# Optimization experiments

Hardware: AMD Instinct MI355X
Metric: run time of the kernel (lower is better)

## Reference

```python
import jax, jax.numpy as jnp
import numpy as np

B, V_IN, V_OUT, F_IN, F_OUT, N_CP = 100000, 128, 128, 512, 512, 16
DIM_H = max(V_IN, V_OUT)  # hidden_vectors=None -> max(dim_vectors_in, dim_vectors_out)
EPS = 1e-8


def setup_inputs() -> dict:
    key = jax.random.key(0)
    ks = jax.random.split(key, 9)
    u = lambda k, shape, scale: jax.random.uniform(k, shape, jnp.float32, -scale, scale)
    wh_k = 1.0 / np.sqrt(V_IN).astype(np.float32)
    wu_k = 1.0 / np.sqrt(DIM_H + N_CP).astype(np.float32)
    f_in = DIM_H + N_CP + F_IN  # 656
    kf = 1.0 / np.sqrt(f_in).astype(np.float32)
    kg = 1.0 / np.sqrt(F_OUT).astype(np.float32)
    return {
        "feats": jax.random.normal(ks[0], (B, F_IN), jnp.float32),
        "vectors": jax.random.normal(ks[1], (B, V_IN, 3), jnp.float32),
        "Wh": u(ks[2], (V_IN, DIM_H), wh_k),
        "Wcp": u(ks[3], (V_IN, 2 * N_CP), wh_k),
        "Wu": u(ks[4], (DIM_H + N_CP, V_OUT), wu_k),
        "Wf": u(ks[5], (f_in, F_OUT), kf),      # torch Linear weight, stored (in,out)
        "bf": u(ks[6], (F_OUT,), kf),
        "Wg": u(ks[7], (F_OUT, V_OUT), kg),
        "bg": u(ks[8], (V_OUT,), kg),
    }


def reference(feats, vectors, Wh, Wcp, Wu, Wf, bf, Wg, bg):
    # vectors: [b, v_in, 3]; mix vector channels (matmul acts per xyz component c)
    Vh = jnp.einsum('bvc,vh->bhc', vectors, Wh)            # [b, dim_h, 3]
    # cross-product features
    Vcp = jnp.einsum('bvc,vp->bpc', vectors, Wcp)          # [b, 2*n_cp, 3]
    cp = jnp.cross(Vcp[:, :N_CP], Vcp[:, N_CP:])           # [b, n_cp, 3]
    Vh = jnp.concatenate([Vh, cp], axis=1)                 # [b, dim_h+n_cp, 3]
    Vu = jnp.einsum('bkc,ko->boc', Vh, Wu)                 # [b, v_out, 3]
    # clamped L2 norm over xyz
    sh = jnp.sqrt(jnp.maximum(jnp.sum(Vh * Vh, axis=-1), EPS))  # [b, dim_h+n_cp]
    s = jnp.concatenate([feats, sh], axis=1)               # [b, dim_h+n_cp+f_in]
    feats_out = jax.nn.silu(s @ Wf + bf)                   # [b, f_out]
    gating = feats_out @ Wg + bg                           # [b, v_out]
    vectors_out = jax.nn.sigmoid(gating)[..., None] * Vu   # [b, v_out, 3]
    return feats_out, vectors_out
```

## Files before the change

### kernel.cpp

```cpp
#include <hip/hip_runtime.h>

#define BATCH 100000
#define M3 300000
#define VECBASE 51200000
#define KP 704

typedef float fl4  __attribute__((ext_vector_type(4)));
typedef float f32x4 __attribute__((ext_vector_type(4)));
typedef short s16x4 __attribute__((ext_vector_type(4)));
typedef short s16x8 __attribute__((ext_vector_type(8)));

__device__ __forceinline__ short f2bf(float f) {
  unsigned int u = __float_as_uint(f);
  u += 0x7fffu + ((u >> 16) & 1u);
  return (short)(u >> 16);
}
__device__ __forceinline__ float bf2f(short s) {
  return __uint_as_float(((unsigned int)(unsigned short)s) << 16);
}
__device__ __forceinline__ s16x8 pack8(fl4 a, fl4 b) {
  s16x8 o;
  o[0] = f2bf(a[0]); o[1] = f2bf(a[1]); o[2] = f2bf(a[2]); o[3] = f2bf(a[3]);
  o[4] = f2bf(b[0]); o[5] = f2bf(b[1]); o[6] = f2bf(b[2]); o[7] = f2bf(b[3]);
  return o;
}
__device__ __forceinline__ void glds16(const void* g, void* l) {
  __builtin_amdgcn_global_load_lds((const __attribute__((address_space(1))) void*)g,
                                   (__attribute__((address_space(3))) void*)l, 16, 0, 0);
}
#define WAITBAR(N) asm volatile("s_waitcnt vmcnt(" #N ")\ns_barrier" ::: "memory")
#define RAWBAR()   asm volatile("s_barrier" ::: "memory")

__global__ __launch_bounds__(256) void prep_w(
    const float* __restrict__ feats, const float* __restrict__ Wh,
    const float* __restrict__ Wcp, const float* __restrict__ Wu,
    const float* __restrict__ Wf, const float* __restrict__ Wg,
    short* __restrict__ Ab, short* __restrict__ WB1, short* __restrict__ WuTp,
    short* __restrict__ WfT, short* __restrict__ WgT) {
  const int tid = blockIdx.x * 256 + threadIdx.x;
  const int stride = gridDim.x * 256;
  for (int i = tid; i < 6400000; i += stride) {
    int b = i >> 6, kk = (i & 63) * 8;
    fl4 v0 = *reinterpret_cast<const fl4*>(&feats[(size_t)b * 512 + kk]);
    fl4 v1 = *reinterpret_cast<const fl4*>(&feats[(size_t)b * 512 + kk + 4]);
    *(s16x8*)&Ab[(size_t)b * KP + kk] = pack8(v0, v1);
  }
  for (int gid = tid; gid < 466944; gid += stride) {
    if (gid < 20480) {
      int n = gid >> 7, k = gid & 127;
      WB1[gid] = f2bf(n < 128 ? Wh[k * 128 + n] : Wcp[k * 32 + (n - 128)]);
    } else if (gid < 40960) {
      int i = gid - 20480;
      int o = i / 160, k = i - o * 160;
      WuTp[i] = k < 144 ? f2bf(Wu[k * 128 + o]) : (short)0;
    } else if (gid < 401408) {
      int i = gid - 40960;
      int n = i / KP, k = i - n * KP;
      WfT[i] = k < 656 ? f2bf(Wf[k * 512 + n]) : (short)0;
    } else {
      int i = gid - 401408;
      int n = i >> 9, k = i & 511;
      WgT[i] = f2bf(Wg[k * 128 + n]);
    }
  }
}

__global__ __launch_bounds__(256) void geo_fused(
    const float* __restrict__ vecs, const short* __restrict__ WB1,
    const short* __restrict__ WuTp, short* __restrict__ Ab,
    short* __restrict__ Vub) {
  __shared__ __align__(16) short U[192 * 168];
  const int t = threadIdx.x;
  const int b0 = blockIdx.x * 64;
  const int row0 = blockIdx.x * 192;

#pragma unroll
  for (int it = 0; it < 8; ++it) {
    int fi = (it * 256 + t) * 12;
    int bl = fi / 384;
    int rem = fi - bl * 384;
    int v0 = rem / 3;
    int b = b0 + bl;
    fl4 x = (fl4){0.f, 0.f, 0.f, 0.f}, y = x, z = x;
    if (b < BATCH) {
      const float* p = &vecs[(size_t)b * 384 + rem];
      x = *(const fl4*)p; y = *(const fl4*)(p + 4); z = *(const fl4*)(p + 8);
    }
    float vc[3][4] = {{x[0], x[3], y[2], z[1]},
                      {x[1], y[0], y[3], z[2]},
                      {x[2], y[1], z[0], z[3]}};
#pragma unroll
    for (int c = 0; c < 3; ++c) {
      int row = bl * 3 + c;
      s16x4 q;
#pragma unroll
      for (int e = 0; e < 4; ++e) q[e] = f2bf(vc[c][e]);
      int off = (row << 8) + (v0 << 1);
      *(s16x4*)((char*)U + (off ^ ((row & 7) << 4))) = q;
    }
  }
  __syncthreads();

  const int lane = t & 63, wv = t >> 6;
  const int wr = wv >> 1, wc = wv & 1;
  const int lr = lane & 15, lk = lane >> 4;

  {
    f32x4 acc[6][5];
#pragma unroll
    for (int i = 0; i < 6; ++i)
#pragma unroll
      for (int j = 0; j < 5; ++j) acc[i][j] = (f32x4){0.f, 0.f, 0.f, 0.f};
#pragma unroll
    for (int kk = 0; kk < 4; ++kk) {
      s16x8 af[6], bq[5];
#pragma unroll
      for (int mi = 0; mi < 6; ++mi) {
        int row = wr * 96 + mi * 16 + lr;
        int off = (row << 8) + (kk << 6) + (lk << 4);
        af[mi] = *(const s16x8*)((const char*)U + (off ^ ((row & 7) << 4)));
      }
#pragma unroll
      for (int ni = 0; ni < 5; ++ni)
        bq[ni] = *reinterpret_cast<const s16x8*>(
            &WB1[(wc * 80 + ni * 16 + lr) * 128 + (kk << 5) + (lk << 3)]);
      __builtin_amdgcn_s_setprio(1);
#pragma unroll
      for (int mi = 0; mi < 6; ++mi)
#pragma unroll
        for (int ni = 0; ni < 5; ++ni)
          acc[mi][ni] = __builtin_amdgcn_mfma_f32_16x16x32_bf16(af[mi], bq[ni], acc[mi][ni], 0, 0, 0);
      __builtin_amdgcn_s_setprio(0);
    }
    __syncthreads();
#pragma unroll
    for (int mi = 0; mi < 6; ++mi)
#pragma unroll
      for (int ni = 0; ni < 5; ++ni) {
        int col = wc * 80 + ni * 16 + lr;
#pragma unroll
        for (int r = 0; r < 4; ++r) {
          int row = wr * 96 + mi * 16 + lk * 4 + r;
          U[row * 168 + col] = f2bf(acc[mi][ni][r]);
        }
      }
  }
  __syncthreads();

  {
    int bl = t >> 2, pj = t & 3;
    int gb = b0 + bl;
    float shcp[4];
#pragma unroll
    for (int q = 0; q < 4; ++q) {
      int p = pj * 4 + q;
      float ax = bf2f(U[(bl * 3 + 0) * 168 + 128 + p]);
      float ay = bf2f(U[(bl * 3 + 1) * 168 + 128 + p]);
      float az = bf2f(U[(bl * 3 + 2) * 168 + 128 + p]);
      float bx = bf2f(U[(bl * 3 + 0) * 168 + 144 + p]);
      float by = bf2f(U[(bl * 3 + 1) * 168 + 144 + p]);
      float bz = bf2f(U[(bl * 3 + 2) * 168 + 144 + p]);
      float cx = ay * bz - az * by;
      float cy = az * bx - ax * bz;
      float cz = ax * by - ay * bx;
      U[(bl * 3 + 0) * 168 + 128 + p] = f2bf(cx);
      U[(bl * 3 + 1) * 168 + 128 + p] = f2bf(cy);
      U[(bl * 3 + 2) * 168 + 128 + p] = f2bf(cz);
      U[(bl * 3 + 0) * 168 + 144 + p] = 0;
      U[(bl * 3 + 1) * 168 + 144 + p] = 0;
      U[(bl * 3 + 2) * 168 + 144 + p] = 0;
      shcp[q] = sqrtf(fmaxf(cx * cx + cy * cy + cz * cz, 1e-8f));
    }
    if (gb < BATCH) {
#pragma unroll
      for (int q = 0; q < 4; ++q)
        Ab[(size_t)gb * KP + 512 + 128 + pj * 4 + q] = f2bf(shcp[q]);
#pragma unroll
      for (int z = 0; z < 12; ++z)
        Ab[(size_t)gb * KP + 512 + 144 + pj * 12 + z] = 0;
    }
  }
  {
    int bl = t >> 2, kq = t & 3;
    int gb = b0 + bl;
    if (gb < BATCH) {
#pragma unroll
      for (int j = 0; j < 4; ++j) {
        int k = kq * 32 + j * 8;
        s16x8 r0 = *(const s16x8*)&U[(bl * 3 + 0) * 168 + k];
        s16x8 r1 = *(const s16x8*)&U[(bl * 3 + 1) * 168 + k];
        s16x8 r2 = *(const s16x8*)&U[(bl * 3 + 2) * 168 + k];
        s16x8 o;
#pragma unroll
        for (int e = 0; e < 8; ++e) {
          float x = bf2f(r0[e]), y = bf2f(r1[e]), z = bf2f(r2[e]);
          o[e] = f2bf(sqrtf(fmaxf(x * x + y * y + z * z, 1e-8f)));
        }
        *(s16x8*)&Ab[(size_t)gb * KP + 512 + k] = o;
      }
    }
  }
  __syncthreads();

  {
    f32x4 acc2[6][4];
#pragma unroll
    for (int i = 0; i < 6; ++i)
#pragma unroll
      for (int j = 0; j < 4; ++j) acc2[i][j] = (f32x4){0.f, 0.f, 0.f, 0.f};
#pragma unroll
    for (int kk = 0; kk < 5; ++kk) {
      s16x8 af[6], bq[4];
#pragma unroll
      for (int mi = 0; mi < 6; ++mi) {
        int row = wr * 96 + mi * 16 + lr;
        af[mi] = *(const s16x8*)&U[row * 168 + (kk << 5) + (lk << 3)];
      }
#pragma unroll
      for (int ni = 0; ni < 4; ++ni)
        bq[ni] = *reinterpret_cast<const s16x8*>(
            &WuTp[(wc * 64 + ni * 16 + lr) * 160 + (kk << 5) + (lk << 3)]);
      __builtin_amdgcn_s_setprio(1);
#pragma unroll
      for (int mi = 0; mi < 6; ++mi)
#pragma unroll
        for (int ni = 0; ni < 4; ++ni)
          acc2[mi][ni] = __builtin_amdgcn_mfma_f32_16x16x32_bf16(af[mi], bq[ni], acc2[mi][ni], 0, 0, 0);
      __builtin_amdgcn_s_setprio(0);
    }
#pragma unroll
    for (int mi = 0; mi < 6; ++mi)
#pragma unroll
      for (int ni = 0; ni < 4; ++ni) {
        int col = wc * 64 + ni * 16 + lr;
#pragma unroll
        for (int r = 0; r < 4; ++r) {
          int row = row0 + wr * 96 + mi * 16 + lk * 4 + r;
          if (row < M3) Vub[(size_t)row * 128 + col] = f2bf(acc2[mi][ni][r]);
        }
      }
  }
}

__global__ __launch_bounds__(256) void gemm_feats(
    const short* __restrict__ Ab, const short* __restrict__ WfT,
    const float* __restrict__ bfv, float* __restrict__ out,
    short* __restrict__ fob) {
  const int bid = blockIdx.x;
  const int swz = (bid & 7) * 391 + (bid >> 3);
  const int mt = swz >> 2, nt = swz & 3;
  const int row0 = mt << 7, n0 = nt << 7;
  const int t = threadIdx.x;
  const int lane = t & 63, wv = t >> 6;
  const int wr = wv >> 1, wc = wv & 1;
  const int lr = lane & 15, lk = lane >> 4;

  __shared__ __align__(16) short As[3][128 * 32];
  __shared__ __align__(16) short Bs[3][128 * 32];

  const short* srcA[2];
  const short* srcB[2];
  int dofs[2];
#pragma unroll
  for (int j = 0; j < 2; ++j) {
    int cid = j * 256 + t;
    int row = cid >> 2, ch = cid & 3;
    int chs = ch ^ ((row >> 1) & 3);
    srcA[j] = &Ab[(size_t)min(row0 + row, BATCH - 1) * KP + chs * 8];
    srcB[j] = &WfT[(size_t)(n0 + row) * KP + chs * 8];
    dofs[j] = cid * 8;
  }

  f32x4 acc[4][4];
#pragma unroll
  for (int i = 0; i < 4; ++i)
#pragma unroll
    for (int j = 0; j < 4; ++j) acc[i][j] = (f32x4){0.f, 0.f, 0.f, 0.f};

  auto STAGE = [&](int buf, int ks) {
    const int k0 = ks << 5;
#pragma unroll
    for (int j = 0; j < 2; ++j) glds16(srcA[j] + k0, &As[buf][dofs[j]]);
#pragma unroll
    for (int j = 0; j < 2; ++j) glds16(srcB[j] + k0, &Bs[buf][dofs[j]]);
  };
  auto COMPUTE = [&](int buf) {
    s16x8 af[4], bq[4];
#pragma unroll
    for (int mi = 0; mi < 4; ++mi) {
      int rw = wr * 64 + mi * 16 + lr;
      af[mi] = *(const s16x8*)&As[buf][rw * 32 + (lk ^ ((rw >> 1) & 3)) * 8];
    }
#pragma unroll
    for (int ni = 0; ni < 4; ++ni) {
      int rw = wc * 64 + ni * 16 + lr;
      bq[ni] = *(const s16x8*)&Bs[buf][rw * 32 + (lk ^ ((rw >> 1) & 3)) * 8];
    }
    __builtin_amdgcn_s_setprio(1);
#pragma unroll
    for (int mi = 0; mi < 4; ++mi)
#pragma unroll
      for (int ni = 0; ni < 4; ++ni)
        acc[mi][ni] = __builtin_amdgcn_mfma_f32_16x16x32_bf16(af[mi], bq[ni], acc[mi][ni], 0, 0, 0);
    __builtin_amdgcn_s_setprio(0);
  };

  STAGE(0, 0);
  STAGE(1, 1);
  for (int ks = 0; ks < 22; ++ks) {
    if (ks + 2 < 22) STAGE((ks + 2) % 3, ks + 2);
    if (ks < 20)      WAITBAR(8);
    else if (ks == 20) WAITBAR(4);
    else               WAITBAR(0);
    COMPUTE(ks % 3);
    RAWBAR();
  }

  float* Ls = (float*)&As[0][0];
#pragma unroll
  for (int g = 0; g < 4; ++g) {
    if (wr == (g >> 1)) {
      int miB = (g & 1) * 2;
#pragma unroll
      for (int m2 = 0; m2 < 2; ++m2) {
#pragma unroll
        for (int ni = 0; ni < 4; ++ni) {
          int colL = wc * 64 + ni * 16 + lr;
          float bb = bfv[n0 + colL];
#pragma unroll
          for (int rr = 0; rr < 4; ++rr) {
            int rowL = m2 * 16 + lk * 4 + rr;
            float x = acc[miB + m2][ni][rr] + bb;
            Ls[rowL * 128 + colL] = x / (1.f + __expf(-x));
          }
        }
      }
    }
    __syncthreads();
    {
      int rowL = t >> 3, seg = t & 7;
      int grow = row0 + g * 32 + rowL;
      if (grow < BATCH) {
        const float* p = &Ls[rowL * 128 + seg * 16];
        fl4 a = *(const fl4*)p, b = *(const fl4*)(p + 4);
        fl4 c = *(const fl4*)(p + 8), d = *(const fl4*)(p + 12);
        float* po = &out[(size_t)grow * 512 + n0 + seg * 16];
        *(fl4*)po = a; *(fl4*)(po + 4) = b; *(fl4*)(po + 8) = c; *(fl4*)(po + 12) = d;
        short* pf = &fob[(size_t)grow * 512 + n0 + seg * 16];
        *(s16x8*)pf = pack8(a, b);
        *(s16x8*)(pf + 8) = pack8(c, d);
      }
    }
    __syncthreads();
  }
}

__global__ __launch_bounds__(256) void gemm_gate(
    const short* __restrict__ fob, const short* __restrict__ WgT,
    const float* __restrict__ bg, const short* __restrict__ Vub,
    float* __restrict__ out) {
  const int bid = blockIdx.x;
  const int xcd = bid & 7, bidx = bid >> 3;
  const int swz = (xcd < 6 ? xcd * 98 : 6 * 98 + (xcd - 6) * 97) + bidx;
  const int row0 = swz << 7;
  const int t = threadIdx.x;
  const int lane = t & 63, wv = t >> 6;
  const int wr = wv >> 1, wc = wv & 1;
  const int lr = lane & 15, lk = lane >> 4;

  __shared__ __align__(16) short As[3][128 * 32];
  __shared__ __align__(16) short Bs[3][128 * 32];

  const short* srcA[2];
  const short* srcB[2];
  int dofs[2];
#pragma unroll
  for (int j = 0; j < 2; ++j) {
    int cid = j * 256 + t;
    int row = cid >> 2, ch = cid & 3;
    int chs = ch ^ ((row >> 1) & 3);
    srcA[j] = &fob[(size_t)min(row0 + row, BATCH - 1) * 512 + chs * 8];
    srcB[j] = &WgT[(size_t)row * 512 + chs * 8];
    dofs[j] = cid * 8;
  }

  f32x4 acc[4][4];
#pragma unroll
  for (int i = 0; i < 4; ++i)
#pragma unroll
    for (int j = 0; j < 4; ++j) acc[i][j] = (f32x4){0.f, 0.f, 0.f, 0.f};

  auto STAGE = [&](int buf, int ks) {
    const int k0 = ks << 5;
#pragma unroll
    for (int j = 0; j < 2; ++j) glds16(srcA[j] + k0, &As[buf][dofs[j]]);
#pragma unroll
    for (int j = 0; j < 2; ++j) glds16(srcB[j] + k0, &Bs[buf][dofs[j]]);
  };
  auto COMPUTE = [&](int buf) {
    s16x8 af[4], bq[4];
#pragma unroll
    for (int mi = 0; mi < 4; ++mi) {
      int rw = wr * 64 + mi * 16 + lr;
      af[mi] = *(const s16x8*)&As[buf][rw * 32 + (lk ^ ((rw >> 1) & 3)) * 8];
    }
#pragma unroll
    for (int ni = 0; ni < 4; ++ni) {
      int rw = wc * 64 + ni * 16 + lr;
      bq[ni] = *(const s16x8*)&Bs[buf][rw * 32 + (lk ^ ((rw >> 1) & 3)) * 8];
    }
    __builtin_amdgcn_s_setprio(1);
#pragma unroll
    for (int mi = 0; mi < 4; ++mi)
#pragma unroll
      for (int ni = 0; ni < 4; ++ni)
        acc[mi][ni] = __builtin_amdgcn_mfma_f32_16x16x32_bf16(af[mi], bq[ni], acc[mi][ni], 0, 0, 0);
    __builtin_amdgcn_s_setprio(0);
  };

  STAGE(0, 0);
  STAGE(1, 1);
  for (int ks = 0; ks < 16; ++ks) {
    if (ks + 2 < 16) STAGE((ks + 2) % 3, ks + 2);
    if (ks < 14)      WAITBAR(8);
    else if (ks == 14) WAITBAR(4);
    else               WAITBAR(0);
    COMPUTE(ks % 3);
    RAWBAR();
  }

#pragma unroll
  for (int ni = 0; ni < 4; ++ni) {
    int col = wc * 64 + ni * 16 + lr;
    float bb = bg[col];
#pragma unroll
    for (int mi = 0; mi < 4; ++mi) {
      int rbase = row0 + wr * 64 + mi * 16 + lk * 4;
#pragma unroll
      for (int rr = 0; rr < 4; ++rr) {
        int gr = rbase + rr;
        if (gr < BATCH) {
          float x = acc[mi][ni][rr] + bb;
          float gate = 1.f / (1.f + __expf(-x));
          size_t vb = (size_t)(3 * gr) * 128 + col;
          float* po = &out[VECBASE + ((size_t)gr * 128 + col) * 3];
          po[0] = gate * bf2f(Vub[vb]);
          po[1] = gate * bf2f(Vub[vb + 128]);
          po[2] = gate * bf2f(Vub[vb + 256]);
        }
      }
    }
  }
}

extern "C" void kernel_launch(void* const* d_in, const int* in_sizes, int n_in,
                              void* d_out, int out_size, void* d_ws, size_t ws_size,
                              hipStream_t stream) {
  const float* feats = (const float*)d_in[0];
  const float* vecs  = (const float*)d_in[1];
  const float* Wh    = (const float*)d_in[2];
  const float* Wcp   = (const float*)d_in[3];
  const float* Wu    = (const float*)d_in[4];
  const float* Wf    = (const float*)d_in[5];
  const float* bfv   = (const float*)d_in[6];
  const float* Wg    = (const float*)d_in[7];
  const float* bg    = (const float*)d_in[8];
  float* out = (float*)d_out;

  char* ws = (char*)d_ws;
  short* Ab   = (short*)ws;
  short* Vub  = (short*)(ws + 140800000);
  short* fob  = (short*)(ws + 217600000);
  short* WfT  = (short*)(ws + 320000000);
  short* WgT  = (short*)(ws + 320720896);
  short* WB1  = (short*)(ws + 320851968);
  short* WuTp = (short*)(ws + 320892928);

  hipLaunchKernelGGL(prep_w,     dim3(2048), dim3(256), 0, stream,
                     feats, Wh, Wcp, Wu, Wf, Wg, Ab, WB1, WuTp, WfT, WgT);
  hipLaunchKernelGGL(geo_fused,  dim3(1563), dim3(256), 0, stream,
                     vecs, WB1, WuTp, Ab, Vub);
  hipLaunchKernelGGL(gemm_feats, dim3(3128), dim3(256), 0, stream,
                     Ab, WfT, bfv, out, fob);
  hipLaunchKernelGGL(gemm_gate,  dim3(782),  dim3(256), 0, stream,
                     fob, WgT, bg, Vub, out);
}
```

Measured before the change: 513.9 us.

## Widen feats GEMM tile to 128x256 with 8 waves, single-buffered LDS

```diff
diff --git a/kernel.cpp b/kernel.cpp
--- a/kernel.cpp
+++ b/kernel.cpp
@@ -242,33 +242,35 @@
   }
 }
 
-__global__ __launch_bounds__(256) void gemm_feats(
+__global__ __launch_bounds__(512, 4) void gemm_feats(
     const short* __restrict__ Ab, const short* __restrict__ WfT,
     const float* __restrict__ bfv, float* __restrict__ out,
     short* __restrict__ fob) {
   const int bid = blockIdx.x;
-  const int swz = (bid & 7) * 391 + (bid >> 3);
-  const int mt = swz >> 2, nt = swz & 3;
-  const int row0 = mt << 7, n0 = nt << 7;
+  const int xcd = bid & 7, bi = bid >> 3;
+  const int swz = (xcd < 4 ? xcd * 196 : 784 + (xcd - 4) * 195) + bi;
+  const int mt = swz >> 1, nt = swz & 1;
+  const int row0 = mt << 7, n0 = nt << 8;
   const int t = threadIdx.x;
   const int lane = t & 63, wv = t >> 6;
-  const int wr = wv >> 1, wc = wv & 1;
+  const int wr = wv >> 2, wc = wv & 3;
   const int lr = lane & 15, lk = lane >> 4;
 
-  __shared__ __align__(16) short As[3][128 * 32];
-  __shared__ __align__(16) short Bs[3][128 * 32];
-
-  const short* srcA[2];
+  __shared__ __align__(16) short S[(128 + 256) * 32];
+  short* As = S;
+  short* Bs = S + 4096;
+
+  const int arow = t >> 2, ach = t & 3;
+  const short* srcA = &Ab[(size_t)min(row0 + arow, BATCH - 1) * KP + (ach ^ ((arow >> 1) & 3)) * 8];
+  const int adof = t * 8;
   const short* srcB[2];
-  int dofs[2];
+  int bdof[2];
 #pragma unroll
   for (int j = 0; j < 2; ++j) {
-    int cid = j * 256 + t;
-    int row = cid >> 2, ch = cid & 3;
-    int chs = ch ^ ((row >> 1) & 3);
-    srcA[j] = &Ab[(size_t)min(row0 + row, BATCH - 1) * KP + chs * 8];
-    srcB[j] = &WfT[(size_t)(n0 + row) * KP + chs * 8];
-    dofs[j] = cid * 8;
+    int cid = j * 512 + t;
+    int brow = cid >> 2, bch = cid & 3;
+    srcB[j] = &WfT[(size_t)(n0 + brow) * KP + (bch ^ ((brow >> 1) & 3)) * 8];
+    bdof[j] = cid * 8;
   }
 
   f32x4 acc[4][4];
@@ -277,24 +279,23 @@
 #pragma unroll
     for (int j = 0; j < 4; ++j) acc[i][j] = (f32x4){0.f, 0.f, 0.f, 0.f};
 
-  auto STAGE = [&](int buf, int ks) {
+  for (int ks = 0; ks < 22; ++ks) {
     const int k0 = ks << 5;
-#pragma unroll
-    for (int j = 0; j < 2; ++j) glds16(srcA[j] + k0, &As[buf][dofs[j]]);
-#pragma unroll
-    for (int j = 0; j < 2; ++j) glds16(srcB[j] + k0, &Bs[buf][dofs[j]]);
-  };
-  auto COMPUTE = [&](int buf) {
+    __syncthreads();
+    glds16(srcA + k0, &As[adof]);
+    glds16(srcB[0] + k0, &Bs[bdof[0]]);
+    glds16(srcB[1] + k0, &Bs[bdof[1]]);
+    __syncthreads();
     s16x8 af[4], bq[4];
 #pragma unroll
     for (int mi = 0; mi < 4; ++mi) {
       int rw = wr * 64 + mi * 16 + lr;
-      af[mi] = *(const s16x8*)&As[buf][rw * 32 + (lk ^ ((rw >> 1) & 3)) * 8];
+      af[mi] = *(const s16x8*)&As[rw * 32 + (lk ^ ((rw >> 1) & 3)) * 8];
     }
 #pragma unroll
     for (int ni = 0; ni < 4; ++ni) {
-      int rw = wc * 64 + ni * 16 + lr;
-      bq[ni] = *(const s16x8*)&Bs[buf][rw * 32 + (lk ^ ((rw >> 1) & 3)) * 8];
+      int rn = wc * 64 + ni * 16 + lr;
+      bq[ni] = *(const s16x8*)&Bs[rn * 32 + (lk ^ ((rn >> 1) & 3)) * 8];
     }
     __builtin_amdgcn_s_setprio(1);
 #pragma unroll
@@ -303,55 +304,37 @@
       for (int ni = 0; ni < 4; ++ni)
         acc[mi][ni] = __builtin_amdgcn_mfma_f32_16x16x32_bf16(af[mi], bq[ni], acc[mi][ni], 0, 0, 0);
     __builtin_amdgcn_s_setprio(0);
-  };
-
-  STAGE(0, 0);
-  STAGE(1, 1);
-  for (int ks = 0; ks < 22; ++ks) {
-    if (ks + 2 < 22) STAGE((ks + 2) % 3, ks + 2);
-    if (ks < 20)      WAITBAR(8);
-    else if (ks == 20) WAITBAR(4);
-    else               WAITBAR(0);
-    COMPUTE(ks % 3);
-    RAWBAR();
-  }
-
-  float* Ls = (float*)&As[0][0];
-#pragma unroll
-  for (int g = 0; g < 4; ++g) {
-    if (wr == (g >> 1)) {
-      int miB = (g & 1) * 2;
-#pragma unroll
-      for (int m2 = 0; m2 < 2; ++m2) {
-#pragma unroll
-        for (int ni = 0; ni < 4; ++ni) {
-          int colL = wc * 64 + ni * 16 + lr;
-          float bb = bfv[n0 + colL];
-#pragma unroll
-          for (int rr = 0; rr < 4; ++rr) {
-            int rowL = m2 * 16 + lk * 4 + rr;
-            float x = acc[miB + m2][ni][rr] + bb;
-            Ls[rowL * 128 + colL] = x / (1.f + __expf(-x));
-          }
+  }
+
+  float* Ls = (float*)S;
+#pragma unroll
+  for (int g = 0; g < 8; ++g) {
+    __syncthreads();
+    if (wr == (g >> 2)) {
+      int mi = g & 3;
+#pragma unroll
+      for (int ni = 0; ni < 4; ++ni) {
+        int colL = wc * 64 + ni * 16 + lr;
+        float bb = bfv[n0 + colL];
+#pragma unroll
+        for (int rr = 0; rr < 4; ++rr) {
+          float x = acc[mi][ni][rr] + bb;
+          Ls[(lk * 4 + rr) * 256 + colL] = x / (1.f + __expf(-x));
         }
       }
     }
     __syncthreads();
     {
-      int rowL = t >> 3, seg = t & 7;
-      int grow = row0 + g * 32 + rowL;
+      int rowL = t >> 5, seg = t & 31;
+      int grow = row0 + g * 16 + rowL;
       if (grow < BATCH) {
-        const float* p = &Ls[rowL * 128 + seg * 16];
+        const float* p = &Ls[rowL * 256 + seg * 8];
         fl4 a = *(const fl4*)p, b = *(const fl4*)(p + 4);
-        fl4 c = *(const fl4*)(p + 8), d = *(const fl4*)(p + 12);
-        float* po = &out[(size_t)grow * 512 + n0 + seg * 16];
-        *(fl4*)po = a; *(fl4*)(po + 4) = b; *(fl4*)(po + 8) = c; *(fl4*)(po + 12) = d;
-        short* pf = &fob[(size_t)grow * 512 + n0 + seg * 16];
-        *(s16x8*)pf = pack8(a, b);
-        *(s16x8*)(pf + 8) = pack8(c, d);
-      }
-    }
-    __syncthreads();
+        float* po = &out[(size_t)grow * 512 + n0 + seg * 8];
+        *(fl4*)po = a; *(fl4*)(po + 4) = b;
+        *(s16x8*)&fob[(size_t)grow * 512 + n0 + seg * 8] = pack8(a, b);
+      }
+    }
   }
 }
 
@@ -480,7 +463,7 @@
                      feats, Wh, Wcp, Wu, Wf, Wg, Ab, WB1, WuTp, WfT, WgT);
   hipLaunchKernelGGL(geo_fused,  dim3(1563), dim3(256), 0, stream,
                      vecs, WB1, WuTp, Ab, Vub);
-  hipLaunchKernelGGL(gemm_feats, dim3(3128), dim3(256), 0, stream,
+  hipLaunchKernelGGL(gemm_feats, dim3(1564), dim3(512), 0, stream,
                      Ab, WfT, bfv, out, fob);
   hipLaunchKernelGGL(gemm_gate,  dim3(782),  dim3(256), 0, stream,
                      fob, WgT, bg, Vub, out);
```

Result: faster. 458.5 us (-10.8%).
